# Optimization experiments

Hardware: AMD Instinct MI355X
Metric: run time of the kernel (lower is better)

The kernel has to match this reference:

```python
import jax, jax.numpy as jnp
import numpy as np

IN_C = 256
INTER_C = 128  # in_channels // reduction_ratio


def setup_inputs() -> dict:
    key = jax.random.key(0)
    ks = jax.random.split(key, 9)
    s = 1.0 / np.sqrt(IN_C)
    si = 1.0 / np.sqrt(INTER_C)
    return {
        "x": jax.random.normal(ks[0], (8, IN_C, 64, 64), dtype=jnp.float32),
        "g_w": jax.random.uniform(ks[1], (INTER_C, IN_C), jnp.float32, -s, s),
        "g_b": jax.random.uniform(ks[2], (INTER_C,), jnp.float32, -s, s),
        "theta_w": jax.random.uniform(ks[3], (INTER_C, IN_C), jnp.float32, -s, s),
        "theta_b": jax.random.uniform(ks[4], (INTER_C,), jnp.float32, -s, s),
        "phi_w": jax.random.uniform(ks[5], (INTER_C, IN_C), jnp.float32, -s, s),
        "phi_b": jax.random.uniform(ks[6], (INTER_C,), jnp.float32, -s, s),
        "W_w": jax.random.uniform(ks[7], (IN_C, INTER_C), jnp.float32, -si, si),
        "W_b": jax.random.uniform(ks[8], (IN_C,), jnp.float32, -si, si),
    }


def _conv1x1(x, w, b):
    # x: [b, cin, h, w]; w: [cout, cin] -> [b, cout, h, w]
    return jnp.einsum('oc,bchw->bohw', w, x) + b[None, :, None, None]


def reference(x, g_w, g_b, theta_w, theta_b, phi_w, phi_b, W_w, W_b):
    b, c, h, w = x.shape
    n = h * w
    g_x = _conv1x1(x, g_w, g_b).reshape(b, INTER_C, n)        # [b, i, n]
    theta_x = _conv1x1(x, theta_w, theta_b).reshape(b, INTER_C, n)
    phi_x = _conv1x1(x, phi_w, phi_b).reshape(b, INTER_C, n)
    # f[b, q, k] = sum_i theta[b, i, q] * phi[b, i, k]
    f = jnp.einsum('biq,bik->bqk', theta_x, phi_x)            # [b, n, n]
    f_div_C = jax.nn.softmax(f, axis=-1)
    # y[b, q, i] = sum_k f_div_C[b, q, k] * g_x[b, i, k]
    y = jnp.einsum('bqk,bik->biq', f_div_C, g_x)              # [b, i, n]
    y = y.reshape(b, INTER_C, h, w)
    W_y = _conv1x1(y, W_w, W_b)
    return W_y + x
```

## Files before the change

kernel.cpp:

```cpp
#include <hip/hip_runtime.h>
#include <hip/hip_bf16.h>
#include <stdint.h>

#define NB 8
#define CIN 256
#define IC 128
#define NP 4096

typedef __attribute__((ext_vector_type(8))) short s8v;
typedef __attribute__((ext_vector_type(4))) short s4v;
typedef __attribute__((ext_vector_type(16))) float f16v;
typedef __attribute__((ext_vector_type(4))) float f4v;

#define MFMA32(a, b, c) __builtin_amdgcn_mfma_f32_32x32x16_bf16(a, b, c, 0, 0, 0)

__device__ __forceinline__ unsigned short f2bf(float f) {
  union { float f; unsigned int u; } v; v.f = f;
  unsigned int u = v.u;
  return (unsigned short)((u + 0x7FFFu + ((u >> 16) & 1u)) >> 16);
}

__device__ __forceinline__ unsigned short f2bf_h(float f) {
  __hip_bfloat16 h = __float2bfloat16(f);
  union { __hip_bfloat16 h; unsigned short u; } cv; cv.h = h;
  return cv.u;
}

__device__ __forceinline__ float bf2f(short s) {
  union { unsigned int u; float f; } cv;
  cv.u = ((unsigned int)(unsigned short)s) << 16;
  return cv.f;
}

typedef const unsigned int __attribute__((address_space(1))) gas_u32;
typedef unsigned int __attribute__((address_space(3))) las_u32;
__device__ __forceinline__ void gload_lds16(const void* g, void* l) {
  __builtin_amdgcn_global_load_lds((gas_u32*)g, (las_u32*)l, 16, 0, 0);
}

__global__ __launch_bounds__(256) void k_transpose(const float* __restrict__ x,
                                                   unsigned short* __restrict__ xT) {
  __shared__ unsigned short T[64][72];
  const int t = threadIdx.x;
  const int b = blockIdx.z;
  const int c0 = blockIdx.y * 64;
  const int p0 = blockIdx.x * 64;
  const float* xp = x + (size_t)b * CIN * NP + (size_t)c0 * NP + p0;
  const int cl = t >> 4;
  const int p4 = (t & 15) * 4;
#pragma unroll
  for (int j = 0; j < 4; ++j) {
    const int c = cl + j * 16;
    const f4v v = *(const f4v*)(xp + (size_t)c * NP + p4);
    ushort4 u;
    u.x = f2bf(v[0]); u.y = f2bf(v[1]); u.z = f2bf(v[2]); u.w = f2bf(v[3]);
    *(ushort4*)&T[c][p4 ^ ((c & 7) * 8)] = u;
  }
  __syncthreads();
  const int p = t >> 2;
  unsigned short* dst = xT + ((size_t)b * NP + p0 + p) * CIN + c0;
#pragma unroll
  for (int half = 0; half < 2; ++half) {
    const int cg = (t & 3) + half * 4;
    alignas(16) unsigned short outv[8];
#pragma unroll
    for (int k = 0; k < 8; ++k)
      outv[k] = T[cg * 8 + k][p ^ (k * 8)];
    *(uint4*)(dst + cg * 8) = *(const uint4*)outv;
  }
}

__global__ __launch_bounds__(256) void k_conv3(const unsigned short* __restrict__ xT,
    const float* __restrict__ thw, const float* __restrict__ thb,
    const float* __restrict__ phw, const float* __restrict__ phb,
    const float* __restrict__ gw,  const float* __restrict__ gb,
    unsigned short* __restrict__ Qg, unsigned short* __restrict__ Kg,
    unsigned short* __restrict__ Vtg) {
  __shared__ unsigned short X[64 * 256];
  const int t = threadIdx.x, lane = t & 63, wid = t >> 6;
  const int b = blockIdx.x & 7;
  const int p0 = (blockIdx.x >> 3) * 64;
  const int hl = lane >> 5;
  const unsigned short* srcb = xT + ((size_t)b * NP + p0) * CIN;
#pragma unroll
  for (int r = 0; r < 8; ++r) {
    const int ci = wid * 512 + r * 64 + lane;
    const int p = ci >> 5, cc = ci & 31;
    gload_lds16(srcb + (size_t)p * CIN + 8 * (cc ^ (2 * (p & 15))),
                (char*)X + wid * 8192 + r * 1024);
  }
  const int orow = wid * 32 + (lane & 31);
  __syncthreads();

  for (int mat = 0; mat < 3; ++mat) {
    const float* W  = (mat == 0) ? thw : ((mat == 1) ? phw : gw);
    const float* Bs = (mat == 0) ? thb : ((mat == 1) ? phb : gb);
    s8v wf[16];
#pragma unroll
    for (int s = 0; s < 16; ++s) {
      const float* wp = W + (size_t)orow * CIN + hl * 8 + 16 * s;
      const f4v a = *(const f4v*)wp;
      const f4v c = *(const f4v*)(wp + 4);
      s8v f;
      f[0] = (short)f2bf(a[0]); f[1] = (short)f2bf(a[1]);
      f[2] = (short)f2bf(a[2]); f[3] = (short)f2bf(a[3]);
      f[4] = (short)f2bf(c[0]); f[5] = (short)f2bf(c[1]);
      f[6] = (short)f2bf(c[2]); f[7] = (short)f2bf(c[3]);
      wf[s] = f;
    }
    float br[16];
#pragma unroll
    for (int r = 0; r < 16; ++r)
      br[r] = Bs[wid * 32 + (r & 3) + 8 * (r >> 2) + 4 * hl];

#pragma unroll
    for (int nt = 0; nt < 2; ++nt) {
      const int p = (lane & 31) + nt * 32;
      f16v acc;
#pragma unroll
      for (int i = 0; i < 16; ++i) acc[i] = 0.f;
#pragma unroll
      for (int s = 0; s < 16; ++s) {
        const int cc0 = hl + 2 * s;
        const s8v xf = *(const s8v*)&X[p * 256 + 8 * (cc0 ^ (2 * (p & 15)))];
        acc = MFMA32(wf[s], xf, acc);
      }
      if (mat < 2) {
        unsigned short* G = ((mat == 0) ? Qg : Kg) + ((size_t)b * NP + p0 + p) * IC;
#pragma unroll
        for (int grp = 0; grp < 4; ++grp) {
          const int d0 = wid * 32 + 8 * grp + 4 * hl;
          ushort4 u;
          u.x = f2bf(acc[grp * 4 + 0] + br[grp * 4 + 0]);
          u.y = f2bf(acc[grp * 4 + 1] + br[grp * 4 + 1]);
          u.z = f2bf(acc[grp * 4 + 2] + br[grp * 4 + 2]);
          u.w = f2bf(acc[grp * 4 + 3] + br[grp * 4 + 3]);
          *(ushort4*)(G + d0) = u;
        }
      } else {
        unsigned short* G = Vtg + (size_t)b * IC * NP + p0 + p;
#pragma unroll
        for (int r = 0; r < 16; ++r) {
          const int row = wid * 32 + (r & 3) + 8 * (r >> 2) + 4 * hl;
          G[(size_t)row * NP] = f2bf(acc[r] + br[r]);
        }
      }
    }
  }
}

__global__ __launch_bounds__(256, 2) void k_attn(const unsigned short* __restrict__ Qg,
    const unsigned short* __restrict__ Kg, const unsigned short* __restrict__ Vtg,
    unsigned short* __restrict__ Opart, float2* __restrict__ stats) {
  __shared__ unsigned short Klds[2][64 * 128];
  __shared__ unsigned short Vlds[2][128 * 68];
  const int t = threadIdx.x, lane = t & 63, wid = t >> 6;
  const int bid = blockIdx.x;
  const int b = bid & 7;
  const int q0 = ((bid >> 3) & 31) * 128;
  const int half = bid >> 8;
  const int it0 = half * 32;
  const int hl = lane >> 5;
  const int q = q0 + wid * 32 + (lane & 31);
  const unsigned short* Qp = Qg + (size_t)b * NP * IC + (size_t)q * IC;
  s8v qf[8];
#pragma unroll
  for (int s = 0; s < 8; ++s) {
    const s8v v = *(const s8v*)(Qp + hl * 8 + 16 * s);
    s8v r;
#pragma unroll
    for (int j = 0; j < 8; ++j)
      r[j] = (short)f2bf_h(bf2f(v[j]) * 1.44269504f);
    qf[s] = r;
  }
  f16v oa[4];
#pragma unroll
  for (int dt = 0; dt < 4; ++dt)
#pragma unroll
    for (int i = 0; i < 16; ++i) oa[dt][i] = 0.f;
  float m = -3.0e38f, lsum = 0.f;
  const unsigned short* Kb = Kg + (size_t)b * NP * IC;
  const unsigned short* Vb = Vtg + (size_t)b * IC * NP;
  const int ch = t & 7, dbase = t >> 3;

  uint4 vreg[4];
#pragma unroll
  for (int r = 0; r < 4; ++r) {
    const int ci = wid * 256 + r * 64 + lane;
    const int kv = ci >> 4, cc = ci & 15;
    gload_lds16(Kb + (size_t)(it0 * 64 + kv) * IC + 8 * (cc ^ (kv & 15)),
                (char*)&Klds[0][0] + wid * 4096 + r * 1024);
  }
  {
    const unsigned short* vs = Vb + it0 * 64 + ch * 8;
#pragma unroll
    for (int j = 0; j < 4; ++j)
      vreg[j] = *(const uint4*)(vs + (size_t)(dbase + j * 32) * NP);
#pragma unroll
    for (int j = 0; j < 4; ++j) {
      uint2* w0 = (uint2*)&Vlds[0][(dbase + j * 32) * 68 + ch * 8];
      w0[0] = make_uint2(vreg[j].x, vreg[j].y);
      w0[1] = make_uint2(vreg[j].z, vreg[j].w);
    }
  }
  __syncthreads();

  for (int it = it0; it < it0 + 32; ++it) {
    const int cur = it & 1;
    const bool more = (it < it0 + 31);
    if (more) {
      const int kv0n = (it + 1) * 64;
      const unsigned short* vs = Vb + kv0n + ch * 8;
#pragma unroll
      for (int j = 0; j < 4; ++j)
        vreg[j] = *(const uint4*)(vs + (size_t)(dbase + j * 32) * NP);
#pragma unroll
      for (int r = 0; r < 4; ++r) {
        const int ci = wid * 256 + r * 64 + lane;
        const int kv = ci >> 4, cc = ci & 15;
        gload_lds16(Kb + (size_t)(kv0n + kv) * IC + 8 * (cc ^ (kv & 15)),
                    (char*)&Klds[cur ^ 1][0] + wid * 4096 + r * 1024);
      }
    }
    f16v st0, st1;
#pragma unroll
    for (int i = 0; i < 16; ++i) { st0[i] = 0.f; st1[i] = 0.f; }
    __builtin_amdgcn_s_setprio(1);
#pragma unroll
    for (int s = 0; s < 8; ++s) {
      const int cc0 = hl + 2 * s;
      const int kva = lane & 31;
      const s8v ka  = *(const s8v*)&Klds[cur][kva * 128 + 8 * (cc0 ^ (kva & 15))];
      const s8v kb2 = *(const s8v*)&Klds[cur][(kva + 32) * 128 + 8 * (cc0 ^ (kva & 15))];
      st0 = MFMA32(ka, qf[s], st0);
      st1 = MFMA32(kb2, qf[s], st1);
    }
    __builtin_amdgcn_s_setprio(0);
    float tm[16];
#pragma unroll
    for (int i = 0; i < 16; ++i) tm[i] = fmaxf(st0[i], st1[i]);
#pragma unroll
    for (int w = 8; w >= 1; w >>= 1)
#pragma unroll
      for (int i = 0; i < 16; ++i) if (i < w) tm[i] = fmaxf(tm[i], tm[i + w]);
    float pmax = fmaxf(tm[0], __shfl_xor(tm[0], 32));
    if (__any(pmax > m + 8.f)) {
      const float mn = fmaxf(m, pmax);
      const float sc = __builtin_amdgcn_exp2f(m - mn);
      m = mn;
      lsum *= sc;
#pragma unroll
      for (int dt = 0; dt < 4; ++dt)
#pragma unroll
        for (int i = 0; i < 16; ++i) oa[dt][i] *= sc;
    }
#pragma unroll
    for (int i = 0; i < 16; ++i) st0[i] = __builtin_amdgcn_exp2f(st0[i] - m);
#pragma unroll
    for (int i = 0; i < 16; ++i) st1[i] = __builtin_amdgcn_exp2f(st1[i] - m);
    float ts[16];
#pragma unroll
    for (int i = 0; i < 16; ++i) ts[i] = st0[i] + st1[i];
#pragma unroll
    for (int w = 8; w >= 1; w >>= 1)
#pragma unroll
      for (int i = 0; i < 16; ++i) if (i < w) ts[i] += ts[i + w];
    lsum += ts[0] + __shfl_xor(ts[0], 32);
    s8v pf0, pf1, pf2, pf3;
#pragma unroll
    for (int i = 0; i < 8; ++i) {
      pf0[i] = (short)f2bf_h(st0[i]);
      pf1[i] = (short)f2bf_h(st0[8 + i]);
      pf2[i] = (short)f2bf_h(st1[i]);
      pf3[i] = (short)f2bf_h(st1[8 + i]);
    }
    if (more) {
#pragma unroll
      for (int j = 0; j < 4; ++j) {
        uint2* w0 = (uint2*)&Vlds[cur ^ 1][(dbase + j * 32) * 68 + ch * 8];
        w0[0] = make_uint2(vreg[j].x, vreg[j].y);
        w0[1] = make_uint2(vreg[j].z, vreg[j].w);
      }
    }
    __builtin_amdgcn_s_setprio(1);
#pragma unroll
    for (int ks = 0; ks < 4; ++ks) {
      const int k0 = 4 * hl + 16 * (ks & 1) + 32 * (ks >> 1);
      const s8v pcur = (ks == 0) ? pf0 : ((ks == 1) ? pf1 : ((ks == 2) ? pf2 : pf3));
#pragma unroll
      for (int dt = 0; dt < 4; ++dt) {
        const int d = dt * 32 + (lane & 31);
        const s4v va = *(const s4v*)&Vlds[cur][d * 68 + k0];
        const s4v vb2 = *(const s4v*)&Vlds[cur][d * 68 + k0 + 8];
        s8v vf;
        vf[0] = va[0]; vf[1] = va[1]; vf[2] = va[2]; vf[3] = va[3];
        vf[4] = vb2[0]; vf[5] = vb2[1]; vf[6] = vb2[2]; vf[7] = vb2[3];
        oa[dt] = MFMA32(vf, pcur, oa[dt]);
      }
    }
    __builtin_amdgcn_s_setprio(0);
    __syncthreads();
  }
  const float inv = 1.0f / lsum;
  unsigned short* Op = Opart + (size_t)half * NB * NP * IC + ((size_t)b * NP + q) * IC;
#pragma unroll
  for (int dt = 0; dt < 4; ++dt) {
#pragma unroll
    for (int grp = 0; grp < 4; ++grp) {
      const int d0 = dt * 32 + 8 * grp + 4 * hl;
      ushort4 u;
      u.x = f2bf_h(oa[dt][grp * 4 + 0] * inv);
      u.y = f2bf_h(oa[dt][grp * 4 + 1] * inv);
      u.z = f2bf_h(oa[dt][grp * 4 + 2] * inv);
      u.w = f2bf_h(oa[dt][grp * 4 + 3] * inv);
      *(ushort4*)(Op + d0) = u;
    }
  }
  if (hl == 0)
    stats[(size_t)half * NB * NP + (size_t)b * NP + q] = make_float2(m, lsum);
}

__global__ __launch_bounds__(256) void k_out(const unsigned short* __restrict__ Opart,
    const float2* __restrict__ stats,
    const float* __restrict__ Ww, const float* __restrict__ Wb,
    const float* __restrict__ x, float* __restrict__ out) {
  __shared__ unsigned short Y[64 * 128];
  const int t = threadIdx.x, lane = t & 63, wid = t >> 6;
  const int b = blockIdx.x & 7;
  const int p0 = (blockIdx.x >> 3) * 64;
  const int mt = blockIdx.y;
  const int hl = lane >> 5;
  {
    const int p = t >> 2;
    const int quarter = t & 3;
    const int ihb = quarter * 32;
    const int gq = p0 + p;
    const float2 s0 = stats[(size_t)b * NP + gq];
    const float2 s1 = stats[(size_t)NB * NP + (size_t)b * NP + gq];
    const float mm = fmaxf(s0.x, s1.x);
    const float w0 = s0.y * exp2f(s0.x - mm);
    const float w1 = s1.y * exp2f(s1.x - mm);
    const float rinv = 1.0f / (w0 + w1);
    const float a0 = w0 * rinv, a1 = w1 * rinv;
    const unsigned short* P0 = Opart + ((size_t)b * NP + gq) * IC + ihb;
    const unsigned short* P1 = Opart + (size_t)NB * NP * IC + ((size_t)b * NP + gq) * IC + ihb;
#pragma unroll
    for (int c8 = 0; c8 < 4; ++c8) {
      const s8v v0 = *(const s8v*)(P0 + c8 * 8);
      const s8v v1 = *(const s8v*)(P1 + c8 * 8);
      alignas(16) unsigned short o[8];
#pragma unroll
      for (int j = 0; j < 8; ++j)
        o[j] = f2bf_h(a0 * bf2f(v0[j]) + a1 * bf2f(v1[j]));
      const int cc = quarter * 4 + c8;
      *(uint4*)&Y[p * 128 + 8 * (cc ^ (p & 15))] = *(const uint4*)o;
    }
  }
  const int orow = mt * 128 + wid * 32 + (lane & 31);
  s8v wf[8];
#pragma unroll
  for (int s = 0; s < 8; ++s) {
    const float* wp = Ww + (size_t)orow * IC + hl * 8 + 16 * s;
    const f4v a = *(const f4v*)wp;
    const f4v c = *(const f4v*)(wp + 4);
    s8v f;
    f[0] = (short)f2bf(a[0]); f[1] = (short)f2bf(a[1]);
    f[2] = (short)f2bf(a[2]); f[3] = (short)f2bf(a[3]);
    f[4] = (short)f2bf(c[0]); f[5] = (short)f2bf(c[1]);
    f[6] = (short)f2bf(c[2]); f[7] = (short)f2bf(c[3]);
    wf[s] = f;
  }
  float br[16];
#pragma unroll
  for (int r = 0; r < 16; ++r)
    br[r] = Wb[mt * 128 + wid * 32 + (r & 3) + 8 * (r >> 2) + 4 * hl];
  __syncthreads();
#pragma unroll
  for (int nt = 0; nt < 2; ++nt) {
    const int p = (lane & 31) + nt * 32;
    f16v acc;
#pragma unroll
    for (int i = 0; i < 16; ++i) acc[i] = 0.f;
#pragma unroll
    for (int s = 0; s < 8; ++s) {
      const int cc0 = hl + 2 * s;
      const s8v yf = *(const s8v*)&Y[p * 128 + 8 * (cc0 ^ (p & 15))];
      acc = MFMA32(wf[s], yf, acc);
    }
    const size_t pidx = (size_t)b * CIN * NP + (size_t)(p0 + p);
#pragma unroll
    for (int r = 0; r < 16; ++r) {
      const int row = mt * 128 + wid * 32 + (r & 3) + 8 * (r >> 2) + 4 * hl;
      const size_t idx = pidx + (size_t)row * NP;
      out[idx] = acc[r] + br[r] + x[idx];
    }
  }
}

extern "C" void kernel_launch(void* const* d_in, const int* in_sizes, int n_in,
                              void* d_out, int out_size, void* d_ws, size_t ws_size,
                              hipStream_t stream) {
  const float* x   = (const float*)d_in[0];
  const float* gw  = (const float*)d_in[1];
  const float* gb  = (const float*)d_in[2];
  const float* thw = (const float*)d_in[3];
  const float* thb = (const float*)d_in[4];
  const float* phw = (const float*)d_in[5];
  const float* phb = (const float*)d_in[6];
  const float* Ww  = (const float*)d_in[7];
  const float* Wb  = (const float*)d_in[8];
  float* out = (float*)d_out;

  unsigned short* ws  = (unsigned short*)d_ws;
  unsigned short* xT  = ws;
  unsigned short* Opart = ws;
  unsigned short* Qg  = ws + 8388608;
  unsigned short* Kg  = Qg + 4194304;
  unsigned short* Vtg = Kg + 4194304;
  float2* stats = (float2*)(Vtg + 4194304);

  k_transpose<<<dim3(64, 4, 8), dim3(256), 0, stream>>>(x, xT);
  k_conv3<<<dim3(512), dim3(256), 0, stream>>>(xT, thw, thb, phw, phb, gw, gb,
                                               Qg, Kg, Vtg);
  k_attn<<<dim3(512), dim3(256), 0, stream>>>(Qg, Kg, Vtg, Opart, stats);
  k_out<<<dim3(512, 2), dim3(256), 0, stream>>>(Opart, stats, Ww, Wb, x, out);
}
```

Before: 152.6 us.

## Fuse fp32-to-bf16 transpose into conv kernel and fold log2e into theta weights

Removes the separate transpose kernel: the conv kernel now reads fp32 x directly, converts it to bf16 and transposes it through a small LDS staging tile into the swizzled X buffer. This drops one launch and the round trip of the bf16 transposed copy of x through global memory. The log2(e) scale for the softmax is folded into the theta weights and bias, so the attention kernel loads Q without rescaling it per element. The trade-off is extra barriers and serial LDS staging inside the conv kernel, and the pre-scale now rounds differently (applied before the bf16 conversion rather than after).

Measured after the change: 151.0 us. About the same (-1.0%).

```diff
diff --git a/kernel.cpp b/kernel.cpp
--- a/kernel.cpp
+++ b/kernel.cpp
@@ -38,63 +38,51 @@
   __builtin_amdgcn_global_load_lds((gas_u32*)g, (las_u32*)l, 16, 0, 0);
 }
 
-__global__ __launch_bounds__(256) void k_transpose(const float* __restrict__ x,
-                                                   unsigned short* __restrict__ xT) {
-  __shared__ unsigned short T[64][72];
-  const int t = threadIdx.x;
-  const int b = blockIdx.z;
-  const int c0 = blockIdx.y * 64;
-  const int p0 = blockIdx.x * 64;
-  const float* xp = x + (size_t)b * CIN * NP + (size_t)c0 * NP + p0;
-  const int cl = t >> 4;
-  const int p4 = (t & 15) * 4;
-#pragma unroll
-  for (int j = 0; j < 4; ++j) {
-    const int c = cl + j * 16;
-    const f4v v = *(const f4v*)(xp + (size_t)c * NP + p4);
-    ushort4 u;
-    u.x = f2bf(v[0]); u.y = f2bf(v[1]); u.z = f2bf(v[2]); u.w = f2bf(v[3]);
-    *(ushort4*)&T[c][p4 ^ ((c & 7) * 8)] = u;
-  }
-  __syncthreads();
-  const int p = t >> 2;
-  unsigned short* dst = xT + ((size_t)b * NP + p0 + p) * CIN + c0;
-#pragma unroll
-  for (int half = 0; half < 2; ++half) {
-    const int cg = (t & 3) + half * 4;
-    alignas(16) unsigned short outv[8];
-#pragma unroll
-    for (int k = 0; k < 8; ++k)
-      outv[k] = T[cg * 8 + k][p ^ (k * 8)];
-    *(uint4*)(dst + cg * 8) = *(const uint4*)outv;
-  }
-}
-
-__global__ __launch_bounds__(256) void k_conv3(const unsigned short* __restrict__ xT,
+__global__ __launch_bounds__(256) void k_conv3(const float* __restrict__ x,
     const float* __restrict__ thw, const float* __restrict__ thb,
     const float* __restrict__ phw, const float* __restrict__ phb,
     const float* __restrict__ gw,  const float* __restrict__ gb,
     unsigned short* __restrict__ Qg, unsigned short* __restrict__ Kg,
     unsigned short* __restrict__ Vtg) {
   __shared__ unsigned short X[64 * 256];
+  __shared__ unsigned short T[64][72];
   const int t = threadIdx.x, lane = t & 63, wid = t >> 6;
   const int b = blockIdx.x & 7;
   const int p0 = (blockIdx.x >> 3) * 64;
   const int hl = lane >> 5;
-  const unsigned short* srcb = xT + ((size_t)b * NP + p0) * CIN;
-#pragma unroll
-  for (int r = 0; r < 8; ++r) {
-    const int ci = wid * 512 + r * 64 + lane;
-    const int p = ci >> 5, cc = ci & 31;
-    gload_lds16(srcb + (size_t)p * CIN + 8 * (cc ^ (2 * (p & 15))),
-                (char*)X + wid * 8192 + r * 1024);
+  const float* xb = x + (size_t)b * CIN * NP + p0;
+  const int cl = t >> 4;
+  const int p4 = (t & 15) * 4;
+  for (int sub = 0; sub < 4; ++sub) {
+    const int c0 = sub * 64;
+#pragma unroll
+    for (int j = 0; j < 4; ++j) {
+      const int cloc = cl + j * 16;
+      const f4v v = *(const f4v*)(xb + (size_t)(c0 + cloc) * NP + p4);
+      ushort4 u;
+      u.x = f2bf(v[0]); u.y = f2bf(v[1]); u.z = f2bf(v[2]); u.w = f2bf(v[3]);
+      *(ushort4*)&T[cloc][p4 ^ ((cloc & 7) * 8)] = u;
+    }
+    __syncthreads();
+    const int p = t >> 2;
+#pragma unroll
+    for (int half = 0; half < 2; ++half) {
+      const int cg = (t & 3) + half * 4;
+      alignas(16) unsigned short outv[8];
+#pragma unroll
+      for (int k = 0; k < 8; ++k)
+        outv[k] = T[cg * 8 + k][p ^ (k * 8)];
+      const int cc = sub * 8 + cg;
+      *(uint4*)&X[p * 256 + 8 * (cc ^ (2 * (p & 15)))] = *(const uint4*)outv;
+    }
+    __syncthreads();
   }
   const int orow = wid * 32 + (lane & 31);
-  __syncthreads();
 
   for (int mat = 0; mat < 3; ++mat) {
     const float* W  = (mat == 0) ? thw : ((mat == 1) ? phw : gw);
     const float* Bs = (mat == 0) ? thb : ((mat == 1) ? phb : gb);
+    const float wsc = (mat == 0) ? 1.44269504f : 1.0f;
     s8v wf[16];
 #pragma unroll
     for (int s = 0; s < 16; ++s) {
@@ -102,16 +90,16 @@
       const f4v a = *(const f4v*)wp;
       const f4v c = *(const f4v*)(wp + 4);
       s8v f;
-      f[0] = (short)f2bf(a[0]); f[1] = (short)f2bf(a[1]);
-      f[2] = (short)f2bf(a[2]); f[3] = (short)f2bf(a[3]);
-      f[4] = (short)f2bf(c[0]); f[5] = (short)f2bf(c[1]);
-      f[6] = (short)f2bf(c[2]); f[7] = (short)f2bf(c[3]);
+      f[0] = (short)f2bf(a[0] * wsc); f[1] = (short)f2bf(a[1] * wsc);
+      f[2] = (short)f2bf(a[2] * wsc); f[3] = (short)f2bf(a[3] * wsc);
+      f[4] = (short)f2bf(c[0] * wsc); f[5] = (short)f2bf(c[1] * wsc);
+      f[6] = (short)f2bf(c[2] * wsc); f[7] = (short)f2bf(c[3] * wsc);
       wf[s] = f;
     }
     float br[16];
 #pragma unroll
     for (int r = 0; r < 16; ++r)
-      br[r] = Bs[wid * 32 + (r & 3) + 8 * (r >> 2) + 4 * hl];
+      br[r] = Bs[wid * 32 + (r & 3) + 8 * (r >> 2) + 4 * hl] * wsc;
 
 #pragma unroll
     for (int nt = 0; nt < 2; ++nt) {
@@ -165,14 +153,8 @@
   const unsigned short* Qp = Qg + (size_t)b * NP * IC + (size_t)q * IC;
   s8v qf[8];
 #pragma unroll
-  for (int s = 0; s < 8; ++s) {
-    const s8v v = *(const s8v*)(Qp + hl * 8 + 16 * s);
-    s8v r;
-#pragma unroll
-    for (int j = 0; j < 8; ++j)
-      r[j] = (short)f2bf_h(bf2f(v[j]) * 1.44269504f);
-    qf[s] = r;
-  }
+  for (int s = 0; s < 8; ++s)
+    qf[s] = *(const s8v*)(Qp + hl * 8 + 16 * s);
   f16v oa[4];
 #pragma unroll
   for (int dt = 0; dt < 4; ++dt)
@@ -412,15 +394,13 @@
   float* out = (float*)d_out;
 
   unsigned short* ws  = (unsigned short*)d_ws;
-  unsigned short* xT  = ws;
   unsigned short* Opart = ws;
   unsigned short* Qg  = ws + 8388608;
   unsigned short* Kg  = Qg + 4194304;
   unsigned short* Vtg = Kg + 4194304;
   float2* stats = (float2*)(Vtg + 4194304);
 
-  k_transpose<<<dim3(64, 4, 8), dim3(256), 0, stream>>>(x, xT);
-  k_conv3<<<dim3(512), dim3(256), 0, stream>>>(xT, thw, thb, phw, phb, gw, gb,
+  k_conv3<<<dim3(512), dim3(256), 0, stream>>>(x, thw, thb, phw, phb, gw, gb,
                                                Qg, Kg, Vtg);
   k_attn<<<dim3(512), dim3(256), 0, stream>>>(Qg, Kg, Vtg, Opart, stats);
   k_out<<<dim3(512, 2), dim3(256), 0, stream>>>(Opart, stats, Ww, Wb, x, out);
```
